# Performance work log

Hardware: AMD Instinct MI355X
Metric: run time of the kernel (lower is better)

## Reference

```python
import jax, jax.numpy as jnp
import numpy as np

D_K = 64
N_HEADS = 16
D_MODEL = 1024


def setup_inputs() -> dict:
    key = jax.random.key(0)
    ks = jax.random.split(key, 12)
    N, T = 2, 2048
    H = D_K * N_HEADS
    s = 1.0 / np.sqrt(D_MODEL)
    inp = {
        "q": jax.random.normal(ks[0], (N, T, D_MODEL), jnp.float32),
        "k": jax.random.normal(ks[1], (N, T, D_MODEL), jnp.float32),
        "v": jax.random.normal(ks[2], (N, T, D_MODEL), jnp.float32),
        "mask": jax.random.randint(ks[3], (N, T), 0, 2, jnp.int32),
        "Wq": jax.random.normal(ks[4], (D_MODEL, H), jnp.float32) * s,
        "bq": jax.random.normal(ks[5], (H,), jnp.float32) * 0.02,
        "Wk": jax.random.normal(ks[6], (D_MODEL, H), jnp.float32) * s,
        "bk": jax.random.normal(ks[7], (H,), jnp.float32) * 0.02,
        "Wv": jax.random.normal(ks[8], (D_MODEL, H), jnp.float32) * s,
        "bv": jax.random.normal(ks[9], (H,), jnp.float32) * 0.02,
        "Wo": jax.random.normal(ks[10], (H, D_MODEL), jnp.float32) * (1.0 / np.sqrt(H)),
        "bo": jax.random.normal(ks[11], (D_MODEL,), jnp.float32) * 0.02,
    }
    return inp


def reference(q, k, v, mask, Wq, bq, Wk, bk, Wv, bv, Wo, bo):
    N, T, _ = q.shape
    # project and split heads: [N, T, H*dk] -> [N, nH, T, dk]
    def split(x):
        return x.reshape(N, T, N_HEADS, D_K).transpose(0, 2, 1, 3)
    qh = split(q @ Wq + bq)
    kh = split(k @ Wk + bk)
    vh = split(v @ Wv + bv)
    scores = jnp.einsum("bhqd,bhkd->bhqk", qh, kh) / np.sqrt(D_K)
    # key padding mask: mask[:, None, None, :] == 0 -> -inf
    scores = jnp.where(mask[:, None, None, :] == 0, -jnp.inf, scores)
    attn = jax.nn.softmax(scores, axis=-1)
    A = jnp.einsum("bhqk,bhkd->bhqd", attn, vh)
    A = A.transpose(0, 2, 1, 3).reshape(N, T, N_HEADS * D_K)
    return A @ Wo + bo
```

## Files before the change

### kernel.cpp

```cpp
#include <hip/hip_runtime.h>

#define T_SEQ 2048
#define DM 1024
#define NH 16
#define DKH 64
#define NB 2
#define M_ROWS (NB * T_SEQ)
#define QSCALE 0.18033688011112042f

using bf16x8 = __attribute__((ext_vector_type(8))) __bf16;
using f32x4  = __attribute__((ext_vector_type(4))) float;
using halfx4 = __attribute__((ext_vector_type(4))) __fp16;
using halfx2 = __attribute__((ext_vector_type(2))) __fp16;

__device__ __forceinline__ short f2bf(float f) {
  unsigned u = __builtin_bit_cast(unsigned, f);
  u += 0x7fffu + ((u >> 16) & 1u);
  return (short)(u >> 16);
}

#if defined(__has_builtin) && __has_builtin(__builtin_amdgcn_cvt_pk_bf16_f32)
using bf16x2 = __attribute__((ext_vector_type(2))) __bf16;
__device__ __forceinline__ short2 pk2(float a, float b) {
  bf16x2 r = __builtin_amdgcn_cvt_pk_bf16_f32(a, b);
  return __builtin_bit_cast(short2, r);
}
#else
__device__ __forceinline__ short2 pk2(float a, float b) {
  short2 r; r.x = f2bf(a); r.y = f2bf(b); return r;
}
#endif

__device__ __forceinline__ short2 pkh(float a, float b) {
  halfx2 r = __builtin_amdgcn_cvt_pkrtz(a, b);
  return __builtin_bit_cast(short2, r);
}

#if defined(__has_builtin) && __has_builtin(__builtin_amdgcn_exp2f)
__device__ __forceinline__ float fexp2(float x) { return __builtin_amdgcn_exp2f(x); }
#else
__device__ __forceinline__ float fexp2(float x) { return exp2f(x); }
#endif

#define MFMA16F16 __builtin_amdgcn_mfma_f32_16x16x16f16

#define GLD16(g, l)                                                            \
  __builtin_amdgcn_global_load_lds(                                            \
      (const __attribute__((address_space(1))) void*)(g),                      \
      (__attribute__((address_space(3))) void*)(l), 16, 0, 0)

__global__ __launch_bounds__(256) void prep_x(
    const float* __restrict__ q, const float* __restrict__ k,
    const float* __restrict__ v, const int* __restrict__ mask,
    short* __restrict__ dst, float* __restrict__ mf) {
  const float* s = blockIdx.z == 0 ? q : (blockIdx.z == 1 ? k : v);
  short* d = dst + (size_t)blockIdx.z * (M_ROWS * DM);
  const int n4 = M_ROWS * DM / 4;
  for (int i = blockIdx.x * 256 + threadIdx.x; i < n4; i += gridDim.x * 256) {
    float4 f = *(const float4*)(s + i * 4);
    short2 a = pk2(f.x, f.y), b = pk2(f.z, f.w);
    short4 o = {a.x, a.y, b.x, b.y};
    *(short4*)(d + i * 4) = o;
  }
  if (blockIdx.z == 0 && blockIdx.x < 4) {
    int i = (blockIdx.x * 256 + threadIdx.x) * 4;
    int4 m = *(const int4*)(mask + i);
    float4 o = {m.x ? 0.f : -1e38f, m.y ? 0.f : -1e38f,
                m.z ? 0.f : -1e38f, m.w ? 0.f : -1e38f};
    *(float4*)(mf + i) = o;
  }
}

__global__ __launch_bounds__(256) void prep_w(
    const float* __restrict__ w0, const float* __restrict__ w1,
    const float* __restrict__ w2, const float* __restrict__ w3,
    short* __restrict__ dst) {
  __shared__ short T[64][72];
  const float* W = blockIdx.z == 0 ? w0 : blockIdx.z == 1 ? w1
                   : blockIdx.z == 2 ? w2 : w3;
  short* D = dst + (size_t)blockIdx.z * (DM * DM);
  const int k0 = blockIdx.x * 64, n0 = blockIdx.y * 64;
  const int r = threadIdx.x >> 2, cs = (threadIdx.x & 3) * 16;
#pragma unroll
  for (int j = 0; j < 4; ++j) {
    float4 f = *(const float4*)(W + (size_t)(k0 + r) * DM + n0 + cs + j * 4);
    short2 a = pk2(f.x, f.y), b = pk2(f.z, f.w);
    short4 o = {a.x, a.y, b.x, b.y};
    *(short4*)&T[r][cs + j * 4] = o;
  }
  __syncthreads();
  short tmp[16];
#pragma unroll
  for (int i = 0; i < 16; ++i) tmp[i] = T[cs + i][r];
  *(int4*)(D + (size_t)(n0 + r) * DM + k0 + cs) = *(const int4*)&tmp[0];
  *(int4*)(D + (size_t)(n0 + r) * DM + k0 + cs + 8) = *(const int4*)&tmp[8];
}

template <int MODE>
__global__ __launch_bounds__(512) void gemm_bt(
    const short* __restrict__ A_, const short* __restrict__ Bt_,
    const float* __restrict__ b0, const float* __restrict__ b1,
    const float* __restrict__ b2, short* __restrict__ Y,
    float* __restrict__ Yf) {
  __shared__ short As[2][4096];
  __shared__ short Bs[2][4096];
  const int z = (MODE == 0) ? blockIdx.z : 0;
  const short* A = A_ + (size_t)z * (M_ROWS * DM);
  const short* Bt = Bt_ + (size_t)z * (DM * DM);
  short* Yz = (MODE == 0) ? (Y + (size_t)z * ((size_t)M_ROWS * DM)) : Y;
  const float* bias = (MODE == 0) ? (z == 0 ? b0 : (z == 1 ? b1 : b2)) : b0;
  const int m0 = blockIdx.x * 128, n0 = blockIdx.y * 128;
  const int tid = threadIdx.x, w = tid >> 6, lane = tid & 63;
  const int quad = lane >> 4, lm = lane & 15, wa = w & 1, wb = w >> 1;

  const short* Ag = A + (size_t)(m0 + w * 16 + lm) * DM + quad * 8;
  const short* Bg = Bt + (size_t)(n0 + w * 16 + lm) * DM + quad * 8;

  f32x4 acc[4][2];
#pragma unroll
  for (int i = 0; i < 4; ++i)
#pragma unroll
    for (int j = 0; j < 2; ++j) acc[i][j] = (f32x4){0.f, 0.f, 0.f, 0.f};

  GLD16(Ag, &As[0][w * 512]);
  GLD16(Bg, &Bs[0][w * 512]);

  for (int kt = 0; kt < DM / 32; ++kt) {
    const int cb = kt & 1;
    __syncthreads();
    if (kt + 1 < DM / 32) {
      GLD16(Ag + (kt + 1) * 32, &As[cb ^ 1][w * 512]);
      GLD16(Bg + (kt + 1) * 32, &Bs[cb ^ 1][w * 512]);
    }
    bf16x8 af[4], bfr[2];
#pragma unroll
    for (int i = 0; i < 4; ++i)
      af[i] = *(const bf16x8*)&As[cb][(wa * 4 + i) * 512 + quad * 128 + lm * 8];
#pragma unroll
    for (int j = 0; j < 2; ++j)
      bfr[j] = *(const bf16x8*)&Bs[cb][(wb * 2 + j) * 512 + quad * 128 + lm * 8];
#pragma unroll
    for (int mi = 0; mi < 4; ++mi)
#pragma unroll
      for (int j = 0; j < 2; ++j)
        acc[mi][j] = __builtin_amdgcn_mfma_f32_16x16x32_bf16(
            af[mi], bfr[j], acc[mi][j], 0, 0, 0);
  }

  if (MODE == 0 && z < 2) {
#pragma unroll
    for (int j = 0; j < 2; ++j) {
      const int f = n0 + (wb * 2 + j) * 16 + lm;
      const float bv = bias[f];
      const int h = f >> 6, dk = f & 63;
#pragma unroll
      for (int mi = 0; mi < 4; ++mi)
#pragma unroll
        for (int r = 0; r < 4; ++r) {
          const int m = m0 + (wa * 4 + mi) * 16 + quad * 4 + r;
          float val = acc[mi][j][r] + bv;
          if (z == 0) val *= QSCALE;
          const int b = m >> 11, tt = m & (T_SEQ - 1);
          Yz[(((size_t)(b * NH + h) << 11) + tt) * DKH + dk] = f2bf(val);
        }
    }
  } else if (MODE == 0) {
#pragma unroll
    for (int j = 0; j < 2; ++j) {
      const int f = n0 + (wb * 2 + j) * 16 + lm;
      const float bv = bias[f];
      const int h = f >> 6, dk = f & 63;
#pragma unroll
      for (int mi = 0; mi < 4; ++mi) {
        const int t = m0 + (wa * 4 + mi) * 16 + quad * 4;
        const int b = t >> 11, tt = t & (T_SEQ - 1);
        short2 a = pkh(acc[mi][j][0] + bv, acc[mi][j][1] + bv);
        short2 c = pkh(acc[mi][j][2] + bv, acc[mi][j][3] + bv);
        short4 o = {a.x, a.y, c.x, c.y};
        *(short4*)(Yz + (((size_t)(b * NH + h) * DKH + dk) << 11) + tt) = o;
      }
    }
  } else {
#pragma unroll
    for (int j = 0; j < 2; ++j) {
      const int n = n0 + (wb * 2 + j) * 16 + lm;
      const float bv = bias[n];
#pragma unroll
      for (int mi = 0; mi < 4; ++mi)
#pragma unroll
        for (int r = 0; r < 4; ++r) {
          const int m = m0 + (wa * 4 + mi) * 16 + quad * 4 + r;
          Yf[(size_t)m * DM + n] = acc[mi][j][r] + bv;
        }
    }
  }
}

__global__ __launch_bounds__(512) void attn_kernel(
    const short* __restrict__ Qh, const short* __restrict__ Kh,
    const short* __restrict__ Vt, const float* __restrict__ mf,
    short* __restrict__ Ao) {
  __shared__ short Ks[2][4096];
  __shared__ short Vs[2][4096];
  const int qt = blockIdx.x, bh = blockIdx.y;
  const int b = bh >> 4, h = bh & (NH - 1);
  const int tid = threadIdx.x, w = tid >> 6, lane = tid & 63;
  const int quad = lane >> 4, lm = lane & 15;
  const size_t base = (size_t)bh * T_SEQ * DKH;
  const float* mp = mf + b * T_SEQ;
  const int q0 = qt * 128 + w * 16;

  const short* qp = Qh + base + (size_t)(q0 + lm) * DKH;
  const bf16x8 qb0 = *(const bf16x8*)(qp + quad * 8);
  const bf16x8 qb1 = *(const bf16x8*)(qp + 32 + quad * 8);

  const int sw = w & 3;
  const bool isV = w >= 4;
  const short* Sg = isV ? (Vt + base + (size_t)(sw * 16 + lm) * T_SEQ + quad * 8)
                        : (Kh + base + (size_t)(sw * 16 + lm) * DKH + quad * 8);

  f32x4 ot[4];
#pragma unroll
  for (int i = 0; i < 4; ++i) ot[i] = (f32x4){0.f, 0.f, 0.f, 0.f};
  float l_part = 0.f;

  {
    short* d0 = isV ? &Vs[0][sw * 1024] : &Ks[0][sw * 1024];
    GLD16(Sg, d0);
    GLD16(Sg + 32, d0 + 512);
  }

  for (int kt = 0; kt < T_SEQ / 64; ++kt) {
    const int cb = kt & 1;
    const int key0 = kt * 64;
    __syncthreads();
    if (kt + 1 < T_SEQ / 64) {
      const int nk = key0 + 64;
      short* d0 = isV ? &Vs[cb ^ 1][sw * 1024] : &Ks[cb ^ 1][sw * 1024];
      const short* s0 = isV ? (Sg + nk) : (Sg + (size_t)nk * DKH);
      GLD16(s0, d0);
      GLD16(s0 + 32, d0 + 512);
    }

    halfx4 pb[4];
#pragma unroll
    for (int nt = 0; nt < 4; ++nt) {
      bf16x8 ka0 = *(const bf16x8*)&Ks[cb][nt * 1024 + quad * 128 + lm * 8];
      bf16x8 ka1 = *(const bf16x8*)&Ks[cb][nt * 1024 + 512 + quad * 128 + lm * 8];
      f32x4 s = (f32x4){0.f, 0.f, 0.f, 0.f};
      s = __builtin_amdgcn_mfma_f32_16x16x32_bf16(ka0, qb0, s, 0, 0, 0);
      s = __builtin_amdgcn_mfma_f32_16x16x32_bf16(ka1, qb1, s, 0, 0, 0);
      const float4 m4 = *(const float4*)(mp + key0 + nt * 16 + quad * 4);
      float p0 = fexp2(s[0] + m4.x);
      float p1 = fexp2(s[1] + m4.y);
      float p2 = fexp2(s[2] + m4.z);
      float p3 = fexp2(s[3] + m4.w);
      l_part += (p0 + p1) + (p2 + p3);
      short2 a = pkh(p0, p1), c = pkh(p2, p3);
      int2 packed = {(int)(unsigned short)a.x | ((int)(unsigned short)a.y << 16),
                     (int)(unsigned short)c.x | ((int)(unsigned short)c.y << 16)};
      pb[nt] = __builtin_bit_cast(halfx4, packed);
    }

#pragma unroll
    for (int nt2 = 0; nt2 < 4; ++nt2) {
#pragma unroll
      for (int nt = 0; nt < 4; ++nt) {
        const int koff = ((nt & 2) ? 512 : 0) + (2 * (nt & 1) + (quad >> 1)) * 128 +
                         lm * 8 + (quad & 1) * 4;
        halfx4 va = *(const halfx4*)&Vs[cb][nt2 * 1024 + koff];
        ot[nt2] = MFMA16F16(va, pb[nt], ot[nt2], 0, 0, 0);
      }
    }
  }
  l_part += __shfl_xor(l_part, 16, 64);
  l_part += __shfl_xor(l_part, 32, 64);
  const float inv = 1.f / l_part;
  const size_t row = (size_t)(b * T_SEQ + q0 + lm) * DM + h * DKH;
#pragma unroll
  for (int nt = 0; nt < 4; ++nt) {
    short2 a = pk2(ot[nt][0] * inv, ot[nt][1] * inv);
    short2 c = pk2(ot[nt][2] * inv, ot[nt][3] * inv);
    short4 o4 = {a.x, a.y, c.x, c.y};
    *(short4*)(Ao + row + nt * 16 + quad * 4) = o4;
  }
}

extern "C" void kernel_launch(void* const* d_in, const int* in_sizes, int n_in,
                              void* d_out, int out_size, void* d_ws, size_t ws_size,
                              hipStream_t stream) {
  const float* q = (const float*)d_in[0];
  const float* k = (const float*)d_in[1];
  const float* v = (const float*)d_in[2];
  const int* mk = (const int*)d_in[3];
  const float* Wq = (const float*)d_in[4];
  const float* bq = (const float*)d_in[5];
  const float* Wk = (const float*)d_in[6];
  const float* bk = (const float*)d_in[7];
  const float* Wv = (const float*)d_in[8];
  const float* bv = (const float*)d_in[9];
  const float* Wo = (const float*)d_in[10];
  const float* bo = (const float*)d_in[11];

  const size_t XE = (size_t)M_ROWS * DM;
  const size_t WE = (size_t)DM * DM;
  short* xb = (short*)d_ws;
  short* Wt = xb + 3 * XE;
  short* Qh = Wt + 4 * WE;
  float* mf = (float*)(Qh + 3 * XE);
  short* Ao = xb;

  prep_x<<<dim3(1024, 1, 3), 256, 0, stream>>>(q, k, v, mk, xb, mf);
  prep_w<<<dim3(16, 16, 4), 256, 0, stream>>>(Wq, Wk, Wv, Wo, Wt);
  gemm_bt<0><<<dim3(M_ROWS / 128, DM / 128, 3), 512, 0, stream>>>(
      xb, Wt, bq, bk, bv, Qh, nullptr);
  attn_kernel<<<dim3(T_SEQ / 128, NB * NH), 512, 0, stream>>>(
      Qh, Qh + XE, Qh + 2 * XE, mf, Ao);
  gemm_bt<1><<<dim3(M_ROWS / 128, DM / 128, 1), 512, 0, stream>>>(
      Ao, Wt + 3 * WE, bo, nullptr, nullptr, nullptr, (float*)d_out);
}
```

Baseline: 291.3 us.

## Split output GEMM into narrower tiles and double attention key block

Moves the output projection into its own kernel with 128x64 tiles, doubling the grid from 256 to 512 blocks so more of the GPU's compute units are busy. The attention kernel now processes 128 keys per iteration instead of 64, halving the number of barriers and loop iterations at the cost of twice the shared memory per block. It also remaps block indices so consecutive blocks cover different batch-heads. The larger LDS footprint may reduce occupancy.

Result: faster. 264.3 us (-9.3%).

```diff
diff --git a/kernel.cpp b/kernel.cpp
--- a/kernel.cpp
+++ b/kernel.cpp
@@ -96,19 +96,17 @@
   *(int4*)(D + (size_t)(n0 + r) * DM + k0 + cs + 8) = *(const int4*)&tmp[8];
 }
 
-template <int MODE>
-__global__ __launch_bounds__(512) void gemm_bt(
+__global__ __launch_bounds__(512) void gemm_qkv(
     const short* __restrict__ A_, const short* __restrict__ Bt_,
     const float* __restrict__ b0, const float* __restrict__ b1,
-    const float* __restrict__ b2, short* __restrict__ Y,
-    float* __restrict__ Yf) {
+    const float* __restrict__ b2, short* __restrict__ Y) {
   __shared__ short As[2][4096];
   __shared__ short Bs[2][4096];
-  const int z = (MODE == 0) ? blockIdx.z : 0;
+  const int z = blockIdx.z;
   const short* A = A_ + (size_t)z * (M_ROWS * DM);
   const short* Bt = Bt_ + (size_t)z * (DM * DM);
-  short* Yz = (MODE == 0) ? (Y + (size_t)z * ((size_t)M_ROWS * DM)) : Y;
-  const float* bias = (MODE == 0) ? (z == 0 ? b0 : (z == 1 ? b1 : b2)) : b0;
+  short* Yz = Y + (size_t)z * ((size_t)M_ROWS * DM);
+  const float* bias = z == 0 ? b0 : (z == 1 ? b1 : b2);
   const int m0 = blockIdx.x * 128, n0 = blockIdx.y * 128;
   const int tid = threadIdx.x, w = tid >> 6, lane = tid & 63;
   const int quad = lane >> 4, lm = lane & 15, wa = w & 1, wb = w >> 1;
@@ -147,7 +145,7 @@
             af[mi], bfr[j], acc[mi][j], 0, 0, 0);
   }
 
-  if (MODE == 0 && z < 2) {
+  if (z < 2) {
 #pragma unroll
     for (int j = 0; j < 2; ++j) {
       const int f = n0 + (wb * 2 + j) * 16 + lm;
@@ -164,7 +162,7 @@
           Yz[(((size_t)(b * NH + h) << 11) + tt) * DKH + dk] = f2bf(val);
         }
     }
-  } else if (MODE == 0) {
+  } else {
 #pragma unroll
     for (int j = 0; j < 2; ++j) {
       const int f = n0 + (wb * 2 + j) * 16 + lm;
@@ -180,19 +178,63 @@
         *(short4*)(Yz + (((size_t)(b * NH + h) * DKH + dk) << 11) + tt) = o;
       }
     }
-  } else {
-#pragma unroll
-    for (int j = 0; j < 2; ++j) {
-      const int n = n0 + (wb * 2 + j) * 16 + lm;
-      const float bv = bias[n];
-#pragma unroll
-      for (int mi = 0; mi < 4; ++mi)
-#pragma unroll
-        for (int r = 0; r < 4; ++r) {
-          const int m = m0 + (wa * 4 + mi) * 16 + quad * 4 + r;
-          Yf[(size_t)m * DM + n] = acc[mi][j][r] + bv;
-        }
-    }
+  }
+}
+
+__global__ __launch_bounds__(512) void gemm_out(
+    const short* __restrict__ A, const short* __restrict__ Bt,
+    const float* __restrict__ bias, float* __restrict__ Yf) {
+  __shared__ short As[2][4096];
+  __shared__ short Bs[2][2048];
+  const int m0 = blockIdx.x * 128, n0 = blockIdx.y * 64;
+  const int tid = threadIdx.x, w = tid >> 6, lane = tid & 63;
+  const int quad = lane >> 4, lm = lane & 15, wa = w & 3, wb = w >> 2;
+
+  const short* Ag = A + (size_t)(m0 + w * 16 + lm) * DM + quad * 8;
+  const short* Bg = Bt + (size_t)(n0 + (w & 3) * 16 + lm) * DM + quad * 8;
+
+  f32x4 acc[2][2];
+#pragma unroll
+  for (int i = 0; i < 2; ++i)
+#pragma unroll
+    for (int j = 0; j < 2; ++j) acc[i][j] = (f32x4){0.f, 0.f, 0.f, 0.f};
+
+  GLD16(Ag, &As[0][w * 512]);
+  if (w < 4) GLD16(Bg, &Bs[0][w * 512]);
+
+  for (int kt = 0; kt < DM / 32; ++kt) {
+    const int cb = kt & 1;
+    __syncthreads();
+    if (kt + 1 < DM / 32) {
+      GLD16(Ag + (kt + 1) * 32, &As[cb ^ 1][w * 512]);
+      if (w < 4) GLD16(Bg + (kt + 1) * 32, &Bs[cb ^ 1][w * 512]);
+    }
+    bf16x8 af[2], bfr[2];
+#pragma unroll
+    for (int i = 0; i < 2; ++i)
+      af[i] = *(const bf16x8*)&As[cb][(wa * 2 + i) * 512 + quad * 128 + lm * 8];
+#pragma unroll
+    for (int j = 0; j < 2; ++j)
+      bfr[j] = *(const bf16x8*)&Bs[cb][(wb * 2 + j) * 512 + quad * 128 + lm * 8];
+#pragma unroll
+    for (int mi = 0; mi < 2; ++mi)
+#pragma unroll
+      for (int j = 0; j < 2; ++j)
+        acc[mi][j] = __builtin_amdgcn_mfma_f32_16x16x32_bf16(
+            af[mi], bfr[j], acc[mi][j], 0, 0, 0);
+  }
+
+#pragma unroll
+  for (int j = 0; j < 2; ++j) {
+    const int n = n0 + (wb * 2 + j) * 16 + lm;
+    const float bv = bias[n];
+#pragma unroll
+    for (int mi = 0; mi < 2; ++mi)
+#pragma unroll
+      for (int r = 0; r < 4; ++r) {
+        const int m = m0 + (wa * 2 + mi) * 16 + quad * 4 + r;
+        Yf[(size_t)m * DM + n] = acc[mi][j][r] + bv;
+      }
   }
 }
 
@@ -200,9 +242,10 @@
     const short* __restrict__ Qh, const short* __restrict__ Kh,
     const short* __restrict__ Vt, const float* __restrict__ mf,
     short* __restrict__ Ao) {
-  __shared__ short Ks[2][4096];
-  __shared__ short Vs[2][4096];
-  const int qt = blockIdx.x, bh = blockIdx.y;
+  __shared__ short Ks[2][8192];
+  __shared__ short Vs[2][8192];
+  const int id = blockIdx.x + gridDim.x * blockIdx.y;
+  const int bh = id & 31, qt = id >> 5;
   const int b = bh >> 4, h = bh & (NH - 1);
   const int tid = threadIdx.x, w = tid >> 6, lane = tid & 63;
   const int quad = lane >> 4, lm = lane & 15;
@@ -216,35 +259,48 @@
 
   const int sw = w & 3;
   const bool isV = w >= 4;
-  const short* Sg = isV ? (Vt + base + (size_t)(sw * 16 + lm) * T_SEQ + quad * 8)
-                        : (Kh + base + (size_t)(sw * 16 + lm) * DKH + quad * 8);
+  const short* Kg = Kh + base + (size_t)(sw * 16 + lm) * DKH + quad * 8;
+  const short* Vg = Vt + base + (size_t)(sw * 16 + lm) * T_SEQ + quad * 8;
 
   f32x4 ot[4];
 #pragma unroll
   for (int i = 0; i < 4; ++i) ot[i] = (f32x4){0.f, 0.f, 0.f, 0.f};
   float l_part = 0.f;
 
-  {
-    short* d0 = isV ? &Vs[0][sw * 1024] : &Ks[0][sw * 1024];
-    GLD16(Sg, d0);
-    GLD16(Sg + 32, d0 + 512);
-  }
-
-  for (int kt = 0; kt < T_SEQ / 64; ++kt) {
+  if (!isV) {
+    GLD16(Kg, &Ks[0][sw * 1024]);
+    GLD16(Kg + 32, &Ks[0][sw * 1024 + 512]);
+    GLD16(Kg + (size_t)64 * DKH, &Ks[0][(sw + 4) * 1024]);
+    GLD16(Kg + (size_t)64 * DKH + 32, &Ks[0][(sw + 4) * 1024 + 512]);
+  } else {
+    GLD16(Vg, &Vs[0][sw * 2048]);
+    GLD16(Vg + 32, &Vs[0][sw * 2048 + 512]);
+    GLD16(Vg + 64, &Vs[0][sw * 2048 + 1024]);
+    GLD16(Vg + 96, &Vs[0][sw * 2048 + 1536]);
+  }
+
+  for (int kt = 0; kt < T_SEQ / 128; ++kt) {
     const int cb = kt & 1;
-    const int key0 = kt * 64;
+    const int key0 = kt * 128;
     __syncthreads();
-    if (kt + 1 < T_SEQ / 64) {
-      const int nk = key0 + 64;
-      short* d0 = isV ? &Vs[cb ^ 1][sw * 1024] : &Ks[cb ^ 1][sw * 1024];
-      const short* s0 = isV ? (Sg + nk) : (Sg + (size_t)nk * DKH);
-      GLD16(s0, d0);
-      GLD16(s0 + 32, d0 + 512);
-    }
-
-    halfx4 pb[4];
-#pragma unroll
-    for (int nt = 0; nt < 4; ++nt) {
+    if (kt + 1 < T_SEQ / 128) {
+      const int nk = key0 + 128;
+      if (!isV) {
+        GLD16(Kg + (size_t)nk * DKH, &Ks[cb ^ 1][sw * 1024]);
+        GLD16(Kg + (size_t)nk * DKH + 32, &Ks[cb ^ 1][sw * 1024 + 512]);
+        GLD16(Kg + (size_t)(nk + 64) * DKH, &Ks[cb ^ 1][(sw + 4) * 1024]);
+        GLD16(Kg + (size_t)(nk + 64) * DKH + 32, &Ks[cb ^ 1][(sw + 4) * 1024 + 512]);
+      } else {
+        GLD16(Vg + nk, &Vs[cb ^ 1][sw * 2048]);
+        GLD16(Vg + nk + 32, &Vs[cb ^ 1][sw * 2048 + 512]);
+        GLD16(Vg + nk + 64, &Vs[cb ^ 1][sw * 2048 + 1024]);
+        GLD16(Vg + nk + 96, &Vs[cb ^ 1][sw * 2048 + 1536]);
+      }
+    }
+
+    halfx4 pb[8];
+#pragma unroll
+    for (int nt = 0; nt < 8; ++nt) {
       bf16x8 ka0 = *(const bf16x8*)&Ks[cb][nt * 1024 + quad * 128 + lm * 8];
       bf16x8 ka1 = *(const bf16x8*)&Ks[cb][nt * 1024 + 512 + quad * 128 + lm * 8];
       f32x4 s = (f32x4){0.f, 0.f, 0.f, 0.f};
@@ -265,10 +321,11 @@
 #pragma unroll
     for (int nt2 = 0; nt2 < 4; ++nt2) {
 #pragma unroll
-      for (int nt = 0; nt < 4; ++nt) {
-        const int koff = ((nt & 2) ? 512 : 0) + (2 * (nt & 1) + (quad >> 1)) * 128 +
-                         lm * 8 + (quad & 1) * 4;
-        halfx4 va = *(const halfx4*)&Vs[cb][nt2 * 1024 + koff];
+      for (int nt = 0; nt < 8; ++nt) {
+        const int key = nt * 16 + quad * 4;
+        const int seg = key >> 5, kis = key & 31;
+        halfx4 va = *(const halfx4*)&Vs[cb][nt2 * 2048 + seg * 512 +
+                                            (kis >> 3) * 128 + lm * 8 + (kis & 7)];
         ot[nt2] = MFMA16F16(va, pb[nt], ot[nt2], 0, 0, 0);
       }
     }
@@ -312,10 +369,10 @@
 
   prep_x<<<dim3(1024, 1, 3), 256, 0, stream>>>(q, k, v, mk, xb, mf);
   prep_w<<<dim3(16, 16, 4), 256, 0, stream>>>(Wq, Wk, Wv, Wo, Wt);
-  gemm_bt<0><<<dim3(M_ROWS / 128, DM / 128, 3), 512, 0, stream>>>(
-      xb, Wt, bq, bk, bv, Qh, nullptr);
+  gemm_qkv<<<dim3(M_ROWS / 128, DM / 128, 3), 512, 0, stream>>>(
+      xb, Wt, bq, bk, bv, Qh);
   attn_kernel<<<dim3(T_SEQ / 128, NB * NH), 512, 0, stream>>>(
       Qh, Qh + XE, Qh + 2 * XE, mf, Ao);
-  gemm_bt<1><<<dim3(M_ROWS / 128, DM / 128, 1), 512, 0, stream>>>(
-      Ao, Wt + 3 * WE, bo, nullptr, nullptr, nullptr, (float*)d_out);
-}
+  gemm_out<<<dim3(M_ROWS / 128, DM / 64), 512, 0, stream>>>(
+      Ao, Wt + 3 * WE, bo, (float*)d_out);
+}
```
